# Performance work log

Hardware: AMD Instinct MI355X
Metric: run time of the kernel (lower is better)

Reference implementation:

```python
import jax, jax.numpy as jnp
import numpy as np

B, T, NA, NV, K, SD, H, E = 128, 64, 10, 16, 4, 512, 256, 32

def _lin(key, fan_in, fan_out):
    k1, k2 = jax.random.split(key)
    s = 1.0 / np.sqrt(fan_in)
    W = jax.random.uniform(k1, (fan_in, fan_out), jnp.float32, -s, s)
    b = jax.random.uniform(k2, (fan_out,), jnp.float32, -s, s)
    return W, b

def setup_inputs() -> dict:
    key = jax.random.key(0)
    ks = jax.random.split(key, 16)
    inp = {
        "qvals": jax.random.normal(ks[0], (B, T, NA), jnp.float32),
        "causal_relations": jax.random.randint(ks[1], (B, T, K, NV), 0, NA, jnp.int32),
        "states": jax.random.normal(ks[2], (B, T, SD), jnp.float32),
    }
    inp["w00_l1_W"], inp["w00_l1_b"] = _lin(ks[3], SD + NV, H)
    inp["w00_l2_W"], inp["w00_l2_b"] = _lin(ks[4], H, K)
    inp["b00_W"], inp["b00_b"] = _lin(ks[5], SD + NV, 1)
    inp["w01_W"], inp["w01_b"] = _lin(ks[6], SD, NA)
    inp["b01_W"], inp["b01_b"] = _lin(ks[7], SD, 1)
    inp["w1_l1_W"], inp["w1_l1_b"] = _lin(ks[8], SD, H)
    inp["w1_l2_W"], inp["w1_l2_b"] = _lin(ks[9], H, (NV + 1) * E)
    inp["b1_W"], inp["b1_b"] = _lin(ks[10], SD, E)
    inp["w2_l1_W"], inp["w2_l1_b"] = _lin(ks[11], SD, H)
    inp["w2_l2_W"], inp["w2_l2_b"] = _lin(ks[12], H, E)
    inp["b2_l1_W"], inp["b2_l1_b"] = _lin(ks[13], SD, E)
    inp["b2_l2_W"], inp["b2_l2_b"] = _lin(ks[14], E, 1)
    return inp

def reference(qvals, causal_relations, states,
              w00_l1_W, w00_l1_b, w00_l2_W, w00_l2_b, b00_W, b00_b,
              w01_W, w01_b, b01_W, b01_b,
              w1_l1_W, w1_l1_b, w1_l2_W, w1_l2_b, b1_W, b1_b,
              w2_l1_W, w2_l1_b, w2_l2_W, w2_l2_b,
              b2_l1_W, b2_l1_b, b2_l2_W, b2_l2_b):
    b, t, na = qvals.shape
    nv = causal_relations.shape[-1]
    sd = states.shape[-1]
    emb = b1_W.shape[1]

    # (b,t,k,nv) -> (b,t,nv,k); gather per-variable selected agent q-values
    cr = jnp.swapaxes(causal_relations, 2, 3)
    gathered = jnp.take_along_axis(qvals[:, :, None, :], cr, axis=-1)  # (b,t,nv,k)

    # Per-variable hypernets. Original builds a one-hot over n_variables but sets
    # var_onehot[variable] = 1, i.e. batch row `variable` becomes all-ones
    # (replicated faithfully). Split the first Linear into state part + onehot part:
    h_base = states @ w00_l1_W[:sd] + w00_l1_b   # (b,t,H)
    h_delta = w00_l1_W[sd:].sum(0)               # (H,)  contribution of all-ones onehot row
    g_base = states @ b00_W[:sd] + b00_b         # (b,t,1)
    g_delta = b00_W[sd:].sum(0)                  # (1,)

    def per_var(v):
        h = jax.nn.relu(h_base.at[v].add(h_delta))
        w0 = h @ w00_l2_W + w00_l2_b             # (b,t,k)
        b0 = g_base.at[v].add(g_delta)[..., 0]   # (b,t)
        return w0, b0

    w00, b00v = jax.vmap(per_var)(jnp.arange(nv))  # (nv,b,t,k), (nv,b,t)

    # group_qval_v = gathered_v @ |w0_v| + b0_v
    group = jnp.einsum('btvk,vbtk->btv', gathered, jnp.abs(w00)) + jnp.moveaxis(b00v, 0, -1)

    # residual agent mix (hyper_w0_1 / hyper_b0_1): plain linear hypernet, no abs in source
    w01 = states @ w01_W + w01_b                 # (b,t,na)
    other = jnp.einsum('bta,bta->bt', qvals, w01) + (states @ b01_W + b01_b)[..., 0]
    gq = jnp.concatenate([group, other[..., None]], axis=-1)  # (b,t,nv+1)

    # QMIX-style two-layer mix with hypernet weights
    w1 = jnp.abs((jax.nn.relu(states @ w1_l1_W + w1_l1_b) @ w1_l2_W + w1_l2_b)
                 .reshape(b, t, nv + 1, emb))
    b1 = states @ b1_W + b1_b                    # (b,t,E)
    hidden = jax.nn.elu(jnp.einsum('btv,btve->bte', gq, w1) + b1)
    w2 = jnp.abs(jax.nn.relu(states @ w2_l1_W + w2_l1_b) @ w2_l2_W + w2_l2_b)  # (b,t,E)
    b2 = jax.nn.relu(states @ b2_l1_W + b2_l1_b) @ b2_l2_W + b2_l2_b           # (b,t,1)
    y = jnp.sum(hidden * w2, axis=-1, keepdims=True) + b2
    return y  # (b,t,1)
```

## Files before the change

kernel.cpp:

```cpp
#include <hip/hip_runtime.h>
#include <hip/hip_bf16.h>


typedef __hip_bfloat16 bf16;
typedef unsigned short ushort_t;
typedef __attribute__((ext_vector_type(8))) short short8;
typedef __attribute__((ext_vector_type(4))) float f32x4;

#define PA_OFF 256
#define PA_TILES 56
#define PB_OFF (PA_OFF + PA_TILES * 16 * 1024)
#define PB_TILES 36
#define FB_OFF (PB_OFF + PB_TILES * 8 * 1024)
#define NCST 2854
#define WS_NEED (size_t)(FB_OFF + NCST * 4 + 64)

#define MFMA16(a, b, c) __builtin_amdgcn_mfma_f32_16x16x32_bf16(a, b, c, 0, 0, 0)

__device__ __forceinline__ float us2f(ushort_t x) {
  unsigned u = ((unsigned)x) << 16; float f; __builtin_memcpy(&f, &u, 4); return f;
}
__device__ __forceinline__ ushort_t f2us(float v) {
  bf16 h = __float2bfloat16(v); ushort_t r; __builtin_memcpy(&r, &h, 2); return r;
}
template <bool F32>
__device__ __forceinline__ float LD(const void* p, int i) {
  if (F32) return ((const float*)p)[i];
  return us2f(((const ushort_t*)p)[i]);
}

__global__ void detect_dtype_kernel(const void* __restrict__ states, int* __restrict__ flag) {
  int tid = threadIdx.x;
  const unsigned short* u = (const unsigned short*)states;
  int bad = 0;
  for (int i = tid; i < 512; i += 64) {
    unsigned short x = u[i];
    int e = (x >> 7) & 0xFF;
    if (e > 140 || (((x & 0x7FFFu) != 0) && e < 100)) bad++;
  }
  for (int off = 32; off; off >>= 1) bad += __shfl_down(bad, off);
  if (tid == 0) *flag = (bad > 20) ? 1 : 0;
}

template <bool F32>
__device__ void prep_body(int gtid, int T, char* ws,
    const void* w00l1W, const void* w00l1b, const void* w00l2W, const void* w00l2b,
    const void* b00W, const void* b00b,
    const void* w01W, const void* w01b, const void* b01W, const void* b01b,
    const void* w1l1W, const void* w1l1b, const void* w1l2W, const void* w1l2b,
    const void* b1W, const void* b1b,
    const void* w2l1W, const void* w2l1b, const void* w2l2W, const void* w2l2b,
    const void* b2l1W, const void* b2l1b, const void* b2l2W, const void* b2l2b) {
  ushort_t* pa = (ushort_t*)(ws + PA_OFF);
  ushort_t* pb = (ushort_t*)(ws + PB_OFF);
  float* cst = (float*)(ws + FB_OFF);
  for (int o = gtid; o < PA_TILES * 16 * 64; o += T) {
    int lane = o & 63, ks = (o >> 6) & 15, t = o >> 10;
    int lm = lane & 15, qq = lane >> 4;
    int n = t * 16 + lm, kbase = ks * 32 + qq * 8;
    ushort_t v[8];
#pragma unroll
    for (int j = 0; j < 8; ++j) {
      int k = kbase + j; float x;
      if (n < 256) x = LD<F32>(w1l1W, k * 256 + n);
      else if (n < 512) x = LD<F32>(w2l1W, k * 256 + n - 256);
      else if (n < 768) x = LD<F32>(w00l1W, k * 256 + n - 512);
      else if (n < 800) x = LD<F32>(b1W, k * 32 + n - 768);
      else if (n < 832) x = LD<F32>(b2l1W, k * 32 + n - 800);
      else if (n < 842) x = LD<F32>(w01W, k * 10 + n - 832);
      else if (n == 842) x = LD<F32>(b00W, k);
      else if (n == 843) x = LD<F32>(b01W, k);
      else x = 0.f;
      v[j] = f2us(x);
    }
    *(short8*)(pa + (size_t)o * 8) = *(short8*)v;
  }
  for (int o = gtid; o < PB_TILES * 8 * 64; o += T) {
    int lane = o & 63, ks = (o >> 6) & 7, t = o >> 9;
    int lm = lane & 15, qq = lane >> 4;
    int n = t * 16 + lm, kbase = ks * 32 + qq * 8;
    ushort_t v[8];
#pragma unroll
    for (int j = 0; j < 8; ++j) {
      int k = kbase + j;
      float x = (n < 544) ? LD<F32>(w1l2W, k * 544 + n) : LD<F32>(w2l2W, k * 32 + n - 544);
      v[j] = f2us(x);
    }
    *(short8*)(pb + (size_t)o * 8) = *(short8*)v;
  }
  for (int i = gtid; i < NCST; i += T) {
    float x;
    if (i < 896) {
      int c = i;
      if (c < 256) x = LD<F32>(w1l1b, c);
      else if (c < 512) x = LD<F32>(w2l1b, c - 256);
      else if (c < 768) x = LD<F32>(w00l1b, c - 512);
      else if (c < 800) x = LD<F32>(b1b, c - 768);
      else if (c < 832) x = LD<F32>(b2l1b, c - 800);
      else if (c < 842) x = LD<F32>(w01b, c - 832);
      else if (c == 842) x = LD<F32>(b00b, 0);
      else if (c == 843) x = LD<F32>(b01b, 0);
      else x = 0.f;
    } else if (i < 1536) {
      int c = i - 896;
      x = (c < 544) ? LD<F32>(w1l2b, c) : (c < 576 ? LD<F32>(w2l2b, c - 544) : 0.f);
    } else if (i < 1792) {
      int j = i - 1536; float s = 0.f;
      for (int z = 0; z < 16; ++z) s += LD<F32>(w00l1W, (512 + z) * 256 + j);
      x = s;
    } else if (i < 2816) x = LD<F32>(w00l2W, i - 1792);
    else if (i < 2820) x = LD<F32>(w00l2b, i - 2816);
    else if (i < 2852) x = LD<F32>(b2l2W, i - 2820);
    else if (i == 2852) x = LD<F32>(b2l2b, 0);
    else { float s = 0.f; for (int z = 0; z < 16; ++z) s += LD<F32>(b00W, 512 + z); x = s; }
    cst[i] = x;
  }
}

__global__ __launch_bounds__(256) void prep_kernel(char* ws,
    const void* w00l1W, const void* w00l1b, const void* w00l2W, const void* w00l2b,
    const void* b00W, const void* b00b,
    const void* w01W, const void* w01b, const void* b01W, const void* b01b,
    const void* w1l1W, const void* w1l1b, const void* w1l2W, const void* w1l2b,
    const void* b1W, const void* b1b,
    const void* w2l1W, const void* w2l1b, const void* w2l2W, const void* w2l2b,
    const void* b2l1W, const void* b2l1b, const void* b2l2W, const void* b2l2b) {
  int gtid = blockIdx.x * 256 + threadIdx.x;
  int T = gridDim.x * 256;
  if (*(const int*)ws)
    prep_body<true>(gtid, T, ws, w00l1W, w00l1b, w00l2W, w00l2b, b00W, b00b,
        w01W, w01b, b01W, b01b, w1l1W, w1l1b, w1l2W, w1l2b, b1W, b1b,
        w2l1W, w2l1b, w2l2W, w2l2b, b2l1W, b2l1b, b2l2W, b2l2b);
  else
    prep_body<false>(gtid, T, ws, w00l1W, w00l1b, w00l2W, w00l2b, b00W, b00b,
        w01W, w01b, b01W, b01b, w1l1W, w1l1b, w1l2W, w1l2b, b1W, b1b,
        w2l1W, w2l1b, w2l2W, w2l2b, b2l1W, b2l1b, b2l2W, b2l2b);
}

struct SmemM {
  union {
    __align__(16) ushort_t sA[16][520];
    __align__(16) ushort_t w1a[16][548];
  } u;
  __align__(16) ushort_t Am1[16][264];
  __align__(16) ushort_t Am2[16][264];
  __align__(16) ushort_t hb[16][264];
  __align__(16) float cst[NCST];
  float b1v[16][32];
  float rbv[16][32];
  float w2v[16][32];
  float w01v[16][12];
  float qv[16][10];
  unsigned char cr[16][64];
  float w0c[16][4], w0s[16][4];
  float gq[16][18];
  float gbv[16], b01v[16];
  float hid[16][33];
};

struct F4 { float x, y, z, w; };

template <bool F32>
__device__ void mixer_body(SmemM& sm, const char* ws, int n0,
    const void* qvals, const int* crel, const void* states, void* out) {
  const int tid = threadIdx.x;
  const int lane = tid & 63, wv = tid >> 6;
  const int q = lane >> 4, lm = lane & 15;
  const int b_blk = n0 >> 6;
  const ushort_t* pa = (const ushort_t*)(ws + PA_OFF);
  const ushort_t* pb = (const ushort_t*)(ws + PB_OFF);
  const float* fsrc = (const float*)(ws + FB_OFF);

  if (F32) {
    const F4* st4 = (const F4*)states;
    for (int fi = tid; fi < 2048; fi += 512) {
      int r = fi >> 7, c4 = fi & 127;
      F4 v = st4[(size_t)(n0 + r) * 128 + c4];
      ushort_t* dst = &sm.u.sA[r][c4 * 4];
      dst[0] = f2us(v.x); dst[1] = f2us(v.y); dst[2] = f2us(v.z); dst[3] = f2us(v.w);
    }
  } else {
    for (int fi = tid; fi < 1024; fi += 512) {
      int r = fi >> 6, c8 = fi & 63;
      *(short8*)&sm.u.sA[r][c8 * 8] =
          *(const short8*)((const ushort_t*)states + (size_t)(n0 + r) * 512 + c8 * 8);
    }
  }
  for (int i = tid; i < 160; i += 512) sm.qv[i / 10][i % 10] = LD<F32>(qvals, (n0 + i / 10) * 10 + i % 10);
  for (int i = tid; i < 1024; i += 512) sm.cr[i >> 6][i & 63] = (unsigned char)crel[n0 * 64 + i];
  for (int i = tid; i < NCST; i += 512) sm.cst[i] = fsrc[i];
  __syncthreads();

  for (int p = wv; p < 28; p += 8) {
    int t0 = 2 * p;
    const ushort_t* b0 = pa + (size_t)t0 * 8192 + lane * 8;
    f32x4 acc0 = {0.f, 0.f, 0.f, 0.f}, acc1 = {0.f, 0.f, 0.f, 0.f};
#pragma unroll
    for (int ks = 0; ks < 16; ++ks) {
      short8 a = *(const short8*)&sm.u.sA[lm][ks * 32 + q * 8];
      short8 f0 = *(const short8*)(b0 + ks * 512);
      short8 f1 = *(const short8*)(b0 + 8192 + ks * 512);
      acc0 = MFMA16(a, f0, acc0);
      acc1 = MFMA16(a, f1, acc1);
    }
#pragma unroll
    for (int h = 0; h < 2; ++h) {
      f32x4 acc = h ? acc1 : acc0;
      int c = (t0 + h) * 16 + lm;
      if (c >= 844) continue;
      float bias = sm.cst[c];
      int rb = q * 4;
      if (c < 256) {
#pragma unroll
        for (int g = 0; g < 4; ++g) { float v = acc[g] + bias; sm.Am1[rb + g][c] = f2us(v > 0.f ? v : 0.f); }
      } else if (c < 512) {
#pragma unroll
        for (int g = 0; g < 4; ++g) { float v = acc[g] + bias; sm.Am2[rb + g][c - 256] = f2us(v > 0.f ? v : 0.f); }
      } else if (c < 768) {
#pragma unroll
        for (int g = 0; g < 4; ++g) sm.hb[rb + g][c - 512] = f2us(acc[g] + bias);
      } else if (c < 800) {
#pragma unroll
        for (int g = 0; g < 4; ++g) sm.b1v[rb + g][c - 768] = acc[g] + bias;
      } else if (c < 832) {
#pragma unroll
        for (int g = 0; g < 4; ++g) { float v = acc[g] + bias; sm.rbv[rb + g][c - 800] = v > 0.f ? v : 0.f; }
      } else if (c < 842) {
#pragma unroll
        for (int g = 0; g < 4; ++g) sm.w01v[rb + g][c - 832] = acc[g] + bias;
      } else if (c == 842) {
#pragma unroll
        for (int g = 0; g < 4; ++g) sm.gbv[rb + g] = acc[g] + bias;
      } else {
#pragma unroll
        for (int g = 0; g < 4; ++g) sm.b01v[rb + g] = acc[g] + bias;
      }
    }
  }
  __syncthreads();

  for (int p = wv; p < 18; p += 8) {
    int t0 = 2 * p;
    const ushort_t* arow = (t0 < 34) ? sm.Am1[lm] : sm.Am2[lm];
    const ushort_t* b0 = pb + (size_t)t0 * 4096 + lane * 8;
    f32x4 acc0 = {0.f, 0.f, 0.f, 0.f}, acc1 = {0.f, 0.f, 0.f, 0.f};
#pragma unroll
    for (int ks = 0; ks < 8; ++ks) {
      short8 a = *(const short8*)(arow + ks * 32 + q * 8);
      short8 f0 = *(const short8*)(b0 + ks * 512);
      short8 f1 = *(const short8*)(b0 + 4096 + ks * 512);
      acc0 = MFMA16(a, f0, acc0);
      acc1 = MFMA16(a, f1, acc1);
    }
#pragma unroll
    for (int h = 0; h < 2; ++h) {
      f32x4 acc = h ? acc1 : acc0;
      int c = (t0 + h) * 16 + lm;
      float bias = sm.cst[896 + c];
      int rb = q * 4;
      if (c < 544) {
#pragma unroll
        for (int g = 0; g < 4; ++g) sm.u.w1a[rb + g][c] = f2us(fabsf(acc[g] + bias));
      } else {
        int e = c - 544;
#pragma unroll
        for (int g = 0; g < 4; ++g) sm.w2v[rb + g][e] = fabsf(acc[g] + bias);
      }
    }
  }
  __syncthreads();

  if (tid < 128) {
    int r = tid >> 3, k = (tid >> 1) & 3, s = tid & 1;
    const float* w2l = sm.cst + 1792;
    float a = 0.f;
    for (int j = 0; j < 256; ++j) {
      float h = us2f(sm.hb[r][j]);
      if (s) h += sm.cst[1536 + j];
      h = h > 0.f ? h : 0.f;
      a = fmaf(h, w2l[j * 4 + k], a);
    }
    a += sm.cst[2816 + k];
    if (s) sm.w0s[r][k] = a; else sm.w0c[r][k] = a;
  }
  __syncthreads();

  if (tid < 256) {
    int r = tid >> 4, v = tid & 15;
    bool sp = (v == b_blk);
    const float* w0 = sp ? sm.w0s[r] : sm.w0c[r];
    float g = sm.gbv[r] + (sp ? sm.cst[2853] : 0.f);
#pragma unroll
    for (int k = 0; k < 4; ++k) {
      int a = sm.cr[r][k * 16 + v];
      g = fmaf(sm.qv[r][a], fabsf(w0[k]), g);
    }
    sm.gq[r][v] = g;
  } else if (tid < 272) {
    int r = tid - 256;
    float o = sm.b01v[r];
#pragma unroll
    for (int a = 0; a < 10; ++a) o = fmaf(sm.qv[r][a], sm.w01v[r][a], o);
    sm.gq[r][16] = o;
  }
  __syncthreads();

  {
    int r = tid >> 5, e = tid & 31;
    float h = sm.b1v[r][e];
#pragma unroll
    for (int v = 0; v < 17; ++v) h = fmaf(sm.gq[r][v], us2f(sm.u.w1a[r][v * 32 + e]), h);
    float hid = h > 0.f ? h : (expf(h) - 1.f);
    sm.hid[r][e] = hid * sm.w2v[r][e] + sm.rbv[r][e] * sm.cst[2820 + e];
  }
  __syncthreads();

  if (tid < 16) {
    float y = sm.cst[2852];
#pragma unroll
    for (int e = 0; e < 32; ++e) y += sm.hid[tid][e];
    if (F32) ((float*)out)[n0 + tid] = y;
    else ((bf16*)out)[n0 + tid] = __float2bfloat16(y);
  }
}

__global__ __launch_bounds__(512, 4) void causal_mixer_mfma(const char* ws,
    const void* qvals, const int* crel, const void* states, void* out) {
  __shared__ SmemM sm;
  int n0 = blockIdx.x * 16;
  if (*(const int*)ws)
    mixer_body<true>(sm, ws, n0, qvals, crel, states, out);
  else
    mixer_body<false>(sm, ws, n0, qvals, crel, states, out);
}

struct SmemF {
  float s[16][516]; float buf[16][258]; float hd[256];
  float q[16][10]; int cr[16][66];
  float w0c[16][4], w0s[16][4]; float gq[16][17];
  float w01[16][10]; float b01[16]; float gb[16]; float gd;
  float hid[16][32]; float w2[16][32]; float rb[16][32];
};

template <bool F32>
__device__ void fb_body(SmemF& sm, int tid, int n0, int b_blk,
    const void* qvals, const int* crel, const void* states,
    const void* w00l1W, const void* w00l1b, const void* w00l2W, const void* w00l2b,
    const void* b00W, const void* b00b,
    const void* w01W, const void* w01b, const void* b01W, const void* b01b,
    const void* w1l1W, const void* w1l1b, const void* w1l2W, const void* w1l2b,
    const void* b1W, const void* b1b,
    const void* w2l1W, const void* w2l1b, const void* w2l2W, const void* w2l2b,
    const void* b2l1W, const void* b2l1b, const void* b2l2W, const void* b2l2b,
    void* out) {
  for (int idx = tid; idx < 16 * 512; idx += 256) {
    int r = idx >> 9, i = idx & 511;
    sm.s[r][i] = LD<F32>(states, (n0 + r) * 512 + i);
  }
  for (int idx = tid; idx < 160; idx += 256) {
    int r = idx / 10, a = idx % 10;
    sm.q[r][a] = LD<F32>(qvals, (n0 + r) * 10 + a);
  }
  for (int idx = tid; idx < 16 * 64; idx += 256) {
    int r = idx >> 6, kv = idx & 63;
    sm.cr[r][kv] = crel[(n0 + r) * 64 + kv];
  }
  if (tid == 0) {
    float gd = 0.f;
    for (int i = 512; i < 528; ++i) gd += LD<F32>(b00W, i);
    sm.gd = gd;
  }
  __syncthreads();
  {
    const int j = tid;
    float hd = 0.f;
    for (int i = 0; i < 16; ++i) hd += LD<F32>(w00l1W, (512 + i) * 256 + j);
    sm.hd[j] = hd;
    float acc[16]; float bj = LD<F32>(w00l1b, j);
#pragma unroll
    for (int r = 0; r < 16; ++r) acc[r] = bj;
    for (int i = 0; i < 512; ++i) {
      float w = LD<F32>(w00l1W, i * 256 + j);
#pragma unroll
      for (int r = 0; r < 16; ++r) acc[r] = fmaf(sm.s[r][i], w, acc[r]);
    }
#pragma unroll
    for (int r = 0; r < 16; ++r) sm.buf[r][j] = acc[r];
  }
  __syncthreads();
  if (tid < 64) {
    int r = tid >> 2, k = tid & 3;
    float aC = 0.f, aS = 0.f;
    for (int j = 0; j < 256; ++j) {
      float hb = sm.buf[r][j];
      float w = LD<F32>(w00l2W, j * 4 + k);
      float hc = hb > 0.f ? hb : 0.f;
      float hbs = hb + sm.hd[j];
      float hsv = hbs > 0.f ? hbs : 0.f;
      aC = fmaf(hc, w, aC); aS = fmaf(hsv, w, aS);
    }
    float bk = LD<F32>(w00l2b, k);
    sm.w0c[r][k] = aC + bk; sm.w0s[r][k] = aS + bk;
  } else if (tid < 224) {
    int p = tid - 64; int r = p / 10, a = p % 10;
    float acc = 0.f;
    for (int i = 0; i < 512; ++i) acc = fmaf(sm.s[r][i], LD<F32>(w01W, i * 10 + a), acc);
    sm.w01[r][a] = acc + LD<F32>(w01b, a);
  } else if (tid < 240) {
    int r = tid - 224;
    float acc = 0.f;
    for (int i = 0; i < 512; ++i) acc = fmaf(sm.s[r][i], LD<F32>(b00W, i), acc);
    sm.gb[r] = acc + LD<F32>(b00b, 0);
  } else {
    int r = tid - 240;
    float acc = 0.f;
    for (int i = 0; i < 512; ++i) acc = fmaf(sm.s[r][i], LD<F32>(b01W, i), acc);
    sm.b01[r] = acc + LD<F32>(b01b, 0);
  }
  __syncthreads();
  {
    int r = tid >> 4, v = tid & 15;
    bool sp = (v == b_blk);
    const float* w0 = sp ? sm.w0s[r] : sm.w0c[r];
    float g = sm.gb[r] + (sp ? sm.gd : 0.f);
#pragma unroll
    for (int k = 0; k < 4; ++k) {
      int a = sm.cr[r][k * 16 + v];
      g = fmaf(sm.q[r][a], fabsf(w0[k]), g);
    }
    sm.gq[r][v] = g;
  }
  if (tid < 16) {
    int r = tid;
    float o = sm.b01[r];
    for (int a = 0; a < 10; ++a) o = fmaf(sm.q[r][a], sm.w01[r][a], o);
    sm.gq[r][16] = o;
  }
  __syncthreads();
  {
    const int j = tid;
    float acc[16]; float bj = LD<F32>(w1l1b, j);
#pragma unroll
    for (int r = 0; r < 16; ++r) acc[r] = bj;
    for (int i = 0; i < 512; ++i) {
      float w = LD<F32>(w1l1W, i * 256 + j);
#pragma unroll
      for (int r = 0; r < 16; ++r) acc[r] = fmaf(sm.s[r][i], w, acc[r]);
    }
#pragma unroll
    for (int r = 0; r < 16; ++r) sm.buf[r][j] = acc[r] > 0.f ? acc[r] : 0.f;
  }
  __syncthreads();
  for (int p = tid; p < 512; p += 256) {
    int r = p >> 5, e = p & 31;
    float acc = 0.f;
    for (int v = 0; v < 17; ++v) {
      int c = v * 32 + e;
      float d = LD<F32>(w1l2b, c);
      for (int j = 0; j < 256; ++j) d = fmaf(sm.buf[r][j], LD<F32>(w1l2W, j * 544 + c), d);
      acc = fmaf(sm.gq[r][v], fabsf(d), acc);
    }
    float b1v = LD<F32>(b1b, e);
    for (int i = 0; i < 512; ++i) b1v = fmaf(sm.s[r][i], LD<F32>(b1W, i * 32 + e), b1v);
    float x = acc + b1v;
    sm.hid[r][e] = x > 0.f ? x : (expf(x) - 1.f);
  }
  __syncthreads();
  {
    const int j = tid;
    float acc[16]; float bj = LD<F32>(w2l1b, j);
#pragma unroll
    for (int r = 0; r < 16; ++r) acc[r] = bj;
    for (int i = 0; i < 512; ++i) {
      float w = LD<F32>(w2l1W, i * 256 + j);
#pragma unroll
      for (int r = 0; r < 16; ++r) acc[r] = fmaf(sm.s[r][i], w, acc[r]);
    }
#pragma unroll
    for (int r = 0; r < 16; ++r) sm.buf[r][j] = acc[r] > 0.f ? acc[r] : 0.f;
  }
  __syncthreads();
  for (int p = tid; p < 512; p += 256) {
    int r = p >> 5, e = p & 31;
    float d = LD<F32>(w2l2b, e);
    for (int j = 0; j < 256; ++j) d = fmaf(sm.buf[r][j], LD<F32>(w2l2W, j * 32 + e), d);
    sm.w2[r][e] = fabsf(d);
    float rb = LD<F32>(b2l1b, e);
    for (int i = 0; i < 512; ++i) rb = fmaf(sm.s[r][i], LD<F32>(b2l1W, i * 32 + e), rb);
    sm.rb[r][e] = rb > 0.f ? rb : 0.f;
  }
  __syncthreads();
  if (tid < 16) {
    int r = tid;
    float y = 0.f;
#pragma unroll
    for (int e = 0; e < 32; ++e) y = fmaf(sm.hid[r][e], sm.w2[r][e], y);
    float b2v = LD<F32>(b2l2b, 0);
#pragma unroll
    for (int e = 0; e < 32; ++e) b2v = fmaf(sm.rb[r][e], LD<F32>(b2l2W, e), b2v);
    float yv = y + b2v;
    if (F32) ((float*)out)[n0 + r] = yv;
    else ((bf16*)out)[n0 + r] = __float2bfloat16(yv);
  }
}

__global__ __launch_bounds__(256) void causal_mixer_fb(
    const void* qvals, const int* crel, const void* states,
    const void* w00l1W, const void* w00l1b, const void* w00l2W, const void* w00l2b,
    const void* b00W, const void* b00b,
    const void* w01W, const void* w01b, const void* b01W, const void* b01b,
    const void* w1l1W, const void* w1l1b, const void* w1l2W, const void* w1l2b,
    const void* b1W, const void* b1b,
    const void* w2l1W, const void* w2l1b, const void* w2l2W, const void* w2l2b,
    const void* b2l1W, const void* b2l1b, const void* b2l2W, const void* b2l2b,
    void* out, const int* flagp) {
  __shared__ SmemF sm;
  const int tid = threadIdx.x;
  const int n0 = blockIdx.x * 16;
  const int b_blk = n0 >> 6;
  if (*flagp)
    fb_body<true>(sm, tid, n0, b_blk, qvals, crel, states, w00l1W, w00l1b, w00l2W, w00l2b,
        b00W, b00b, w01W, w01b, b01W, b01b, w1l1W, w1l1b, w1l2W, w1l2b, b1W, b1b,
        w2l1W, w2l1b, w2l2W, w2l2b, b2l1W, b2l1b, b2l2W, b2l2b, out);
  else
    fb_body<false>(sm, tid, n0, b_blk, qvals, crel, states, w00l1W, w00l1b, w00l2W, w00l2b,
        b00W, b00b, w01W, w01b, b01W, b01b, w1l1W, w1l1b, w1l2W, w1l2b, b1W, b1b,
        w2l1W, w2l1b, w2l2W, w2l2b, b2l1W, b2l1b, b2l2W, b2l2b, out);
}

extern "C" void kernel_launch(void* const* d_in, const int* in_sizes, int n_in,
                              void* d_out, int out_size, void* d_ws, size_t ws_size,
                              hipStream_t stream) {
  char* ws = (char*)d_ws;
  hipLaunchKernelGGL(detect_dtype_kernel, dim3(1), dim3(64), 0, stream, d_in[2], (int*)ws);
  if (ws_size >= WS_NEED) {
    hipLaunchKernelGGL(prep_kernel, dim3(256), dim3(256), 0, stream, ws,
        d_in[3], d_in[4], d_in[5], d_in[6], d_in[7], d_in[8],
        d_in[9], d_in[10], d_in[11], d_in[12],
        d_in[13], d_in[14], d_in[15], d_in[16], d_in[17], d_in[18],
        d_in[19], d_in[20], d_in[21], d_in[22], d_in[23], d_in[24],
        d_in[25], d_in[26]);
    hipLaunchKernelGGL(causal_mixer_mfma, dim3(512), dim3(512), 0, stream, ws,
        d_in[0], (const int*)d_in[1], d_in[2], d_out);
  } else {
    hipLaunchKernelGGL(causal_mixer_fb, dim3(512), dim3(256), 0, stream,
        d_in[0], (const int*)d_in[1], d_in[2],
        d_in[3], d_in[4], d_in[5], d_in[6], d_in[7], d_in[8],
        d_in[9], d_in[10], d_in[11], d_in[12],
        d_in[13], d_in[14], d_in[15], d_in[16], d_in[17], d_in[18],
        d_in[19], d_in[20], d_in[21], d_in[22], d_in[23], d_in[24],
        d_in[25], d_in[26],
        d_out, (const int*)ws);
  }
}
```

Baseline: 170.3 us.

## Process 32 rows per block with fragment-ordered smem and inline dtype detect

Doubles the rows each mixer block handles (32 instead of 16, grid halved), so every packed weight fragment loaded from global memory feeds two MFMAs, halving weight traffic per row. States and first-layer activations are stored in shared memory already in MFMA fragment order to avoid strided LDS reads. The separate dtype-detect kernel launch is removed and each kernel detects dtype inline. The cost is a larger shared-memory footprint, lower occupancy (launch bounds 512,2), and fewer blocks to spread across CUs.

```diff
diff --git a/kernel.cpp b/kernel.cpp
--- a/kernel.cpp
+++ b/kernel.cpp
@@ -7,13 +7,13 @@
 typedef __attribute__((ext_vector_type(8))) short short8;
 typedef __attribute__((ext_vector_type(4))) float f32x4;
 
-#define PA_OFF 256
+#define PA_OFF 0
 #define PA_TILES 56
-#define PB_OFF (PA_OFF + PA_TILES * 16 * 1024)
+#define PB_OFF (PA_TILES * 16 * 64 * 8 * 2)
 #define PB_TILES 36
-#define FB_OFF (PB_OFF + PB_TILES * 8 * 1024)
+#define FB_OFF (PB_OFF + PB_TILES * 8 * 64 * 8 * 2)
 #define NCST 2854
-#define WS_NEED (size_t)(FB_OFF + NCST * 4 + 64)
+#define WS_NEED (size_t)(FB_OFF + NCST * 4 + 32)
 
 #define MFMA16(a, b, c) __builtin_amdgcn_mfma_f32_16x16x32_bf16(a, b, c, 0, 0, 0)
 
@@ -29,17 +29,17 @@
   return us2f(((const ushort_t*)p)[i]);
 }
 
-__global__ void detect_dtype_kernel(const void* __restrict__ states, int* __restrict__ flag) {
-  int tid = threadIdx.x;
+__device__ __forceinline__ int detect_f32(const void* states) {
   const unsigned short* u = (const unsigned short*)states;
+  int lane = threadIdx.x & 63;
   int bad = 0;
-  for (int i = tid; i < 512; i += 64) {
+  for (int i = lane; i < 512; i += 64) {
     unsigned short x = u[i];
     int e = (x >> 7) & 0xFF;
     if (e > 140 || (((x & 0x7FFFu) != 0) && e < 100)) bad++;
   }
   for (int off = 32; off; off >>= 1) bad += __shfl_down(bad, off);
-  if (tid == 0) *flag = (bad > 20) ? 1 : 0;
+  return __shfl(bad, 0) > 20;
 }
 
 template <bool F32>
@@ -57,35 +57,37 @@
   for (int o = gtid; o < PA_TILES * 16 * 64; o += T) {
     int lane = o & 63, ks = (o >> 6) & 15, t = o >> 10;
     int lm = lane & 15, qq = lane >> 4;
-    int n = t * 16 + lm, kbase = ks * 32 + qq * 8;
+    int n = t * 16 + lm, kb = ks * 32 + qq * 8;
+    const void* src; int stride, nn;
+    if (n < 256)       { src = w1l1W;  stride = 256; nn = n; }
+    else if (n < 512)  { src = w2l1W;  stride = 256; nn = n - 256; }
+    else if (n < 768)  { src = w00l1W; stride = 256; nn = n - 512; }
+    else if (n < 800)  { src = b1W;    stride = 32;  nn = n - 768; }
+    else if (n < 832)  { src = b2l1W;  stride = 32;  nn = n - 800; }
+    else if (n < 842)  { src = w01W;   stride = 10;  nn = n - 832; }
+    else if (n == 842) { src = b00W;   stride = 1;   nn = 0; }
+    else if (n == 843) { src = b01W;   stride = 1;   nn = 0; }
+    else               { src = nullptr; stride = 0;  nn = 0; }
     ushort_t v[8];
-#pragma unroll
-    for (int j = 0; j < 8; ++j) {
-      int k = kbase + j; float x;
-      if (n < 256) x = LD<F32>(w1l1W, k * 256 + n);
-      else if (n < 512) x = LD<F32>(w2l1W, k * 256 + n - 256);
-      else if (n < 768) x = LD<F32>(w00l1W, k * 256 + n - 512);
-      else if (n < 800) x = LD<F32>(b1W, k * 32 + n - 768);
-      else if (n < 832) x = LD<F32>(b2l1W, k * 32 + n - 800);
-      else if (n < 842) x = LD<F32>(w01W, k * 10 + n - 832);
-      else if (n == 842) x = LD<F32>(b00W, k);
-      else if (n == 843) x = LD<F32>(b01W, k);
-      else x = 0.f;
-      v[j] = f2us(x);
+    if (src) {
+#pragma unroll
+      for (int j = 0; j < 8; ++j) v[j] = f2us(LD<F32>(src, (kb + j) * stride + nn));
+    } else {
+#pragma unroll
+      for (int j = 0; j < 8; ++j) v[j] = 0;
     }
     *(short8*)(pa + (size_t)o * 8) = *(short8*)v;
   }
   for (int o = gtid; o < PB_TILES * 8 * 64; o += T) {
     int lane = o & 63, ks = (o >> 6) & 7, t = o >> 9;
     int lm = lane & 15, qq = lane >> 4;
-    int n = t * 16 + lm, kbase = ks * 32 + qq * 8;
+    int n = t * 16 + lm, kb = ks * 32 + qq * 8;
+    const void* src; int stride, nn;
+    if (n < 544) { src = w1l2W; stride = 544; nn = n; }
+    else         { src = w2l2W; stride = 32;  nn = n - 544; }
     ushort_t v[8];
 #pragma unroll
-    for (int j = 0; j < 8; ++j) {
-      int k = kbase + j;
-      float x = (n < 544) ? LD<F32>(w1l2W, k * 544 + n) : LD<F32>(w2l2W, k * 32 + n - 544);
-      v[j] = f2us(x);
-    }
+    for (int j = 0; j < 8; ++j) v[j] = f2us(LD<F32>(src, (kb + j) * stride + nn));
     *(short8*)(pb + (size_t)o * 8) = *(short8*)v;
   }
   for (int i = gtid; i < NCST; i += T) {
@@ -117,7 +119,7 @@
   }
 }
 
-__global__ __launch_bounds__(256) void prep_kernel(char* ws,
+__global__ __launch_bounds__(256) void prep_kernel(char* ws, const void* states,
     const void* w00l1W, const void* w00l1b, const void* w00l2W, const void* w00l2b,
     const void* b00W, const void* b00b,
     const void* w01W, const void* w01b, const void* b01W, const void* b01b,
@@ -127,7 +129,7 @@
     const void* b2l1W, const void* b2l1b, const void* b2l2W, const void* b2l2b) {
   int gtid = blockIdx.x * 256 + threadIdx.x;
   int T = gridDim.x * 256;
-  if (*(const int*)ws)
+  if (detect_f32(states))
     prep_body<true>(gtid, T, ws, w00l1W, w00l1b, w00l2W, w00l2b, b00W, b00b,
         w01W, w01b, b01W, b01b, w1l1W, w1l1b, w1l2W, w1l2b, b1W, b1b,
         w2l1W, w2l1b, w2l2W, w2l2b, b2l1W, b2l1b, b2l2W, b2l2b);
@@ -139,26 +141,26 @@
 
 struct SmemM {
   union {
-    __align__(16) ushort_t sA[16][520];
-    __align__(16) ushort_t w1a[16][548];
+    __align__(16) ushort_t sA[2][8192];
+    __align__(16) ushort_t w1a[32][548];
   } u;
-  __align__(16) ushort_t Am1[16][264];
-  __align__(16) ushort_t Am2[16][264];
-  __align__(16) ushort_t hb[16][264];
+  __align__(16) ushort_t Am1[2][4096];
+  __align__(16) ushort_t Am2[2][4096];
+  __align__(16) ushort_t hb[32][264];
   __align__(16) float cst[NCST];
-  float b1v[16][32];
-  float rbv[16][32];
-  float w2v[16][32];
-  float w01v[16][12];
-  float qv[16][10];
-  unsigned char cr[16][64];
-  float w0c[16][4], w0s[16][4];
-  float gq[16][18];
-  float gbv[16], b01v[16];
-  float hid[16][33];
+  float b1v[32][32];
+  float rbv[32][32];
+  float w2v[32][32];
+  float w01v[32][12];
+  float qv[32][10];
+  unsigned char cr[32][64];
+  float w0c[32][4], w0s[32][4];
+  float gq[32][18];
+  float gbv[32], b01v[32];
+  float hid[32][33];
 };
 
-struct F4 { float x, y, z, w; };
+struct __align__(16) F4 { float x, y, z, w; };
 
 template <bool F32>
 __device__ void mixer_body(SmemM& sm, const char* ws, int n0,
@@ -171,93 +173,104 @@
   const ushort_t* pb = (const ushort_t*)(ws + PB_OFF);
   const float* fsrc = (const float*)(ws + FB_OFF);
 
-  if (F32) {
-    const F4* st4 = (const F4*)states;
-    for (int fi = tid; fi < 2048; fi += 512) {
-      int r = fi >> 7, c4 = fi & 127;
-      F4 v = st4[(size_t)(n0 + r) * 128 + c4];
-      ushort_t* dst = &sm.u.sA[r][c4 * 4];
-      dst[0] = f2us(v.x); dst[1] = f2us(v.y); dst[2] = f2us(v.z); dst[3] = f2us(v.w);
-    }
-  } else {
-    for (int fi = tid; fi < 1024; fi += 512) {
-      int r = fi >> 6, c8 = fi & 63;
-      *(short8*)&sm.u.sA[r][c8 * 8] =
-          *(const short8*)((const ushort_t*)states + (size_t)(n0 + r) * 512 + c8 * 8);
-    }
-  }
-  for (int i = tid; i < 160; i += 512) sm.qv[i / 10][i % 10] = LD<F32>(qvals, (n0 + i / 10) * 10 + i % 10);
-  for (int i = tid; i < 1024; i += 512) sm.cr[i >> 6][i & 63] = (unsigned char)crel[n0 * 64 + i];
+  for (int fi = tid; fi < 2048; fi += 512) {
+    int ln = fi & 63, ks = (fi >> 6) & 15, G = fi >> 10;
+    int l = ln & 15, qq = ln >> 4;
+    int row = G * 16 + l, col = ks * 32 + qq * 8;
+    ushort_t v[8];
+    if (F32) {
+      const F4* p = (const F4*)((const float*)states + (size_t)(n0 + row) * 512 + col);
+      F4 v0 = p[0], v1 = p[1];
+      v[0] = f2us(v0.x); v[1] = f2us(v0.y); v[2] = f2us(v0.z); v[3] = f2us(v0.w);
+      v[4] = f2us(v1.x); v[5] = f2us(v1.y); v[6] = f2us(v1.z); v[7] = f2us(v1.w);
+      *(short8*)&sm.u.sA[G][(size_t)(ks * 64 + ln) * 8] = *(short8*)v;
+    } else {
+      *(short8*)&sm.u.sA[G][(size_t)(ks * 64 + ln) * 8] =
+          *(const short8*)((const ushort_t*)states + (size_t)(n0 + row) * 512 + col);
+    }
+  }
+  for (int i = tid; i < 320; i += 512) sm.qv[i / 10][i % 10] = LD<F32>(qvals, (n0 + i / 10) * 10 + i % 10);
+  for (int i = tid; i < 2048; i += 512) sm.cr[i >> 6][i & 63] = (unsigned char)crel[n0 * 64 + i];
   for (int i = tid; i < NCST; i += 512) sm.cst[i] = fsrc[i];
   __syncthreads();
 
   for (int p = wv; p < 28; p += 8) {
     int t0 = 2 * p;
     const ushort_t* b0 = pa + (size_t)t0 * 8192 + lane * 8;
-    f32x4 acc0 = {0.f, 0.f, 0.f, 0.f}, acc1 = {0.f, 0.f, 0.f, 0.f};
+    f32x4 a00 = {0,0,0,0}, a01 = {0,0,0,0}, a10 = {0,0,0,0}, a11 = {0,0,0,0};
 #pragma unroll
     for (int ks = 0; ks < 16; ++ks) {
-      short8 a = *(const short8*)&sm.u.sA[lm][ks * 32 + q * 8];
+      short8 x0 = *(const short8*)&sm.u.sA[0][(ks * 64 + lane) * 8];
+      short8 x1 = *(const short8*)&sm.u.sA[1][(ks * 64 + lane) * 8];
       short8 f0 = *(const short8*)(b0 + ks * 512);
       short8 f1 = *(const short8*)(b0 + 8192 + ks * 512);
-      acc0 = MFMA16(a, f0, acc0);
-      acc1 = MFMA16(a, f1, acc1);
+      a00 = MFMA16(x0, f0, a00); a10 = MFMA16(x1, f0, a10);
+      a01 = MFMA16(x0, f1, a01); a11 = MFMA16(x1, f1, a11);
     }
 #pragma unroll
     for (int h = 0; h < 2; ++h) {
-      f32x4 acc = h ? acc1 : acc0;
       int c = (t0 + h) * 16 + lm;
       if (c >= 844) continue;
       float bias = sm.cst[c];
-      int rb = q * 4;
-      if (c < 256) {
-#pragma unroll
-        for (int g = 0; g < 4; ++g) { float v = acc[g] + bias; sm.Am1[rb + g][c] = f2us(v > 0.f ? v : 0.f); }
-      } else if (c < 512) {
-#pragma unroll
-        for (int g = 0; g < 4; ++g) { float v = acc[g] + bias; sm.Am2[rb + g][c - 256] = f2us(v > 0.f ? v : 0.f); }
-      } else if (c < 768) {
-#pragma unroll
-        for (int g = 0; g < 4; ++g) sm.hb[rb + g][c - 512] = f2us(acc[g] + bias);
-      } else if (c < 800) {
-#pragma unroll
-        for (int g = 0; g < 4; ++g) sm.b1v[rb + g][c - 768] = acc[g] + bias;
-      } else if (c < 832) {
-#pragma unroll
-        for (int g = 0; g < 4; ++g) { float v = acc[g] + bias; sm.rbv[rb + g][c - 800] = v > 0.f ? v : 0.f; }
-      } else if (c < 842) {
-#pragma unroll
-        for (int g = 0; g < 4; ++g) sm.w01v[rb + g][c - 832] = acc[g] + bias;
-      } else if (c == 842) {
-#pragma unroll
-        for (int g = 0; g < 4; ++g) sm.gbv[rb + g] = acc[g] + bias;
-      } else {
-#pragma unroll
-        for (int g = 0; g < 4; ++g) sm.b01v[rb + g] = acc[g] + bias;
+      int ks2 = (c & 255) >> 5, q2 = (c >> 3) & 3, j2 = c & 7;
+#pragma unroll
+      for (int G = 0; G < 2; ++G) {
+        f32x4 acc = h ? (G ? a11 : a01) : (G ? a10 : a00);
+        int rb = G * 16 + q * 4;
+        if (c < 256) {
+#pragma unroll
+          for (int g = 0; g < 4; ++g) {
+            float v = acc[g] + bias;
+            sm.Am1[G][(ks2 * 64 + q2 * 16 + q * 4 + g) * 8 + j2] = f2us(v > 0.f ? v : 0.f);
+          }
+        } else if (c < 512) {
+#pragma unroll
+          for (int g = 0; g < 4; ++g) {
+            float v = acc[g] + bias;
+            sm.Am2[G][(ks2 * 64 + q2 * 16 + q * 4 + g) * 8 + j2] = f2us(v > 0.f ? v : 0.f);
+          }
+        } else if (c < 768) {
+#pragma unroll
+          for (int g = 0; g < 4; ++g) sm.hb[rb + g][c - 512] = f2us(acc[g] + bias);
+        } else if (c < 800) {
+#pragma unroll
+          for (int g = 0; g < 4; ++g) sm.b1v[rb + g][c - 768] = acc[g] + bias;
+        } else if (c < 832) {
+#pragma unroll
+          for (int g = 0; g < 4; ++g) { float v = acc[g] + bias; sm.rbv[rb + g][c - 800] = v > 0.f ? v : 0.f; }
+        } else if (c < 842) {
+#pragma unroll
+          for (int g = 0; g < 4; ++g) sm.w01v[rb + g][c - 832] = acc[g] + bias;
+        } else if (c == 842) {
+#pragma unroll
+          for (int g = 0; g < 4; ++g) sm.gbv[rb + g] = acc[g] + bias;
+        } else {
+#pragma unroll
+          for (int g = 0; g < 4; ++g) sm.b01v[rb + g] = acc[g] + bias;
+        }
       }
     }
   }
   __syncthreads();
 
-  for (int p = wv; p < 18; p += 8) {
-    int t0 = 2 * p;
-    const ushort_t* arow = (t0 < 34) ? sm.Am1[lm] : sm.Am2[lm];
-    const ushort_t* b0 = pb + (size_t)t0 * 4096 + lane * 8;
-    f32x4 acc0 = {0.f, 0.f, 0.f, 0.f}, acc1 = {0.f, 0.f, 0.f, 0.f};
+  for (int t = wv; t < 36; t += 8) {
+    const ushort_t* A0 = (t < 34) ? sm.Am1[0] : sm.Am2[0];
+    const ushort_t* A1 = (t < 34) ? sm.Am1[1] : sm.Am2[1];
+    const ushort_t* b0 = pb + (size_t)t * 4096 + lane * 8;
+    f32x4 c0 = {0,0,0,0}, c1 = {0,0,0,0};
 #pragma unroll
     for (int ks = 0; ks < 8; ++ks) {
-      short8 a = *(const short8*)(arow + ks * 32 + q * 8);
-      short8 f0 = *(const short8*)(b0 + ks * 512);
-      short8 f1 = *(const short8*)(b0 + 4096 + ks * 512);
-      acc0 = MFMA16(a, f0, acc0);
-      acc1 = MFMA16(a, f1, acc1);
-    }
-#pragma unroll
-    for (int h = 0; h < 2; ++h) {
-      f32x4 acc = h ? acc1 : acc0;
-      int c = (t0 + h) * 16 + lm;
-      float bias = sm.cst[896 + c];
-      int rb = q * 4;
+      short8 x0 = *(const short8*)(A0 + (ks * 64 + lane) * 8);
+      short8 x1 = *(const short8*)(A1 + (ks * 64 + lane) * 8);
+      short8 f = *(const short8*)(b0 + ks * 512);
+      c0 = MFMA16(x0, f, c0); c1 = MFMA16(x1, f, c1);
+    }
+    int c = t * 16 + lm;
+    float bias = sm.cst[896 + c];
+#pragma unroll
+    for (int G = 0; G < 2; ++G) {
+      f32x4 acc = G ? c1 : c0;
+      int rb = G * 16 + q * 4;
       if (c < 544) {
 #pragma unroll
         for (int g = 0; g < 4; ++g) sm.u.w1a[rb + g][c] = f2us(fabsf(acc[g] + bias));
@@ -270,22 +283,22 @@
   }
   __syncthreads();
 
-  if (tid < 128) {
+  if (tid < 256) {
     int r = tid >> 3, k = (tid >> 1) & 3, s = tid & 1;
-    const float* w2l = sm.cst + 1792;
+    const float* wl = sm.cst + 1792;
     float a = 0.f;
     for (int j = 0; j < 256; ++j) {
       float h = us2f(sm.hb[r][j]);
       if (s) h += sm.cst[1536 + j];
       h = h > 0.f ? h : 0.f;
-      a = fmaf(h, w2l[j * 4 + k], a);
+      a = fmaf(h, wl[j * 4 + k], a);
     }
     a += sm.cst[2816 + k];
     if (s) sm.w0s[r][k] = a; else sm.w0c[r][k] = a;
   }
   __syncthreads();
 
-  if (tid < 256) {
+  {
     int r = tid >> 4, v = tid & 15;
     bool sp = (v == b_blk);
     const float* w0 = sp ? sm.w0s[r] : sm.w0c[r];
@@ -296,17 +309,17 @@
       g = fmaf(sm.qv[r][a], fabsf(w0[k]), g);
     }
     sm.gq[r][v] = g;
-  } else if (tid < 272) {
-    int r = tid - 256;
-    float o = sm.b01v[r];
-#pragma unroll
-    for (int a = 0; a < 10; ++a) o = fmaf(sm.qv[r][a], sm.w01v[r][a], o);
-    sm.gq[r][16] = o;
-  }
-  __syncthreads();
-
-  {
-    int r = tid >> 5, e = tid & 31;
+  }
+  if (tid < 32) {
+    float o = sm.b01v[tid];
+#pragma unroll
+    for (int a = 0; a < 10; ++a) o = fmaf(sm.qv[tid][a], sm.w01v[tid][a], o);
+    sm.gq[tid][16] = o;
+  }
+  __syncthreads();
+
+  for (int p = tid; p < 1024; p += 512) {
+    int r = p >> 5, e = p & 31;
     float h = sm.b1v[r][e];
 #pragma unroll
     for (int v = 0; v < 17; ++v) h = fmaf(sm.gq[r][v], us2f(sm.u.w1a[r][v * 32 + e]), h);
@@ -315,7 +328,7 @@
   }
   __syncthreads();
 
-  if (tid < 16) {
+  if (tid < 32) {
     float y = sm.cst[2852];
 #pragma unroll
     for (int e = 0; e < 32; ++e) y += sm.hid[tid][e];
@@ -324,11 +337,11 @@
   }
 }
 
-__global__ __launch_bounds__(512, 4) void causal_mixer_mfma(const char* ws,
+__global__ __launch_bounds__(512, 2) void causal_mixer_mfma(const char* ws,
     const void* qvals, const int* crel, const void* states, void* out) {
   __shared__ SmemM sm;
-  int n0 = blockIdx.x * 16;
-  if (*(const int*)ws)
+  int n0 = blockIdx.x * 32;
+  if (detect_f32(states))
     mixer_body<true>(sm, ws, n0, qvals, crel, states, out);
   else
     mixer_body<false>(sm, ws, n0, qvals, crel, states, out);
@@ -513,12 +526,12 @@
     const void* b1W, const void* b1b,
     const void* w2l1W, const void* w2l1b, const void* w2l2W, const void* w2l2b,
     const void* b2l1W, const void* b2l1b, const void* b2l2W, const void* b2l2b,
-    void* out, const int* flagp) {
+    void* out) {
   __shared__ SmemF sm;
   const int tid = threadIdx.x;
   const int n0 = blockIdx.x * 16;
   const int b_blk = n0 >> 6;
-  if (*flagp)
+  if (detect_f32(states))
     fb_body<true>(sm, tid, n0, b_blk, qvals, crel, states, w00l1W, w00l1b, w00l2W, w00l2b,
         b00W, b00b, w01W, w01b, b01W, b01b, w1l1W, w1l1b, w1l2W, w1l2b, b1W, b1b,
         w2l1W, w2l1b, w2l2W, w2l2b, b2l1W, b2l1b, b2l2W, b2l2b, out);
@@ -532,15 +545,14 @@
                               void* d_out, int out_size, void* d_ws, size_t ws_size,
                               hipStream_t stream) {
   char* ws = (char*)d_ws;
-  hipLaunchKernelGGL(detect_dtype_kernel, dim3(1), dim3(64), 0, stream, d_in[2], (int*)ws);
   if (ws_size >= WS_NEED) {
-    hipLaunchKernelGGL(prep_kernel, dim3(256), dim3(256), 0, stream, ws,
+    hipLaunchKernelGGL(prep_kernel, dim3(256), dim3(256), 0, stream, ws, d_in[2],
         d_in[3], d_in[4], d_in[5], d_in[6], d_in[7], d_in[8],
         d_in[9], d_in[10], d_in[11], d_in[12],
         d_in[13], d_in[14], d_in[15], d_in[16], d_in[17], d_in[18],
         d_in[19], d_in[20], d_in[21], d_in[22], d_in[23], d_in[24],
         d_in[25], d_in[26]);
-    hipLaunchKernelGGL(causal_mixer_mfma, dim3(512), dim3(512), 0, stream, ws,
+    hipLaunchKernelGGL(causal_mixer_mfma, dim3(256), dim3(512), 0, stream, ws,
         d_in[0], (const int*)d_in[1], d_in[2], d_out);
   } else {
     hipLaunchKernelGGL(causal_mixer_fb, dim3(512), dim3(256), 0, stream,
@@ -550,6 +562,6 @@
         d_in[13], d_in[14], d_in[15], d_in[16], d_in[17], d_in[18],
         d_in[19], d_in[20], d_in[21], d_in[22], d_in[23], d_in[24],
         d_in[25], d_in[26],
-        d_out, (const int*)ws);
-  }
-}
+        d_out);
+  }
+}
```

Result: no change. 173.6 us (+1.9%).
